# Optimization experiments

Hardware: AMD Instinct MI355X
Metric: run time of the kernel (lower is better)

## Reference

```python
import jax, jax.numpy as jnp
import numpy as np

EPS = 1e-6

B, R, S, CSEM = 4, 16384, 48, 4


def setup_inputs() -> dict:
    key = jax.random.key(0)
    k1, k2, k3, k4, k5 = jax.random.split(key, 5)
    colors = jax.random.uniform(k1, (B, R, S, 3), dtype=jnp.float32)
    densities = jax.random.normal(k2, (B, R, S, 1), dtype=jnp.float32)
    # depths must be monotonically increasing along the sample axis
    depths = jnp.sort(jax.random.uniform(k3, (B, R, S, 1), dtype=jnp.float32) * 5.0 + 0.5, axis=2)
    # semantics: per-sample class probabilities in [0,1]
    semantics = jax.nn.softmax(jax.random.normal(k4, (B, R, S, CSEM), dtype=jnp.float32), axis=-1)
    levels = jax.random.randint(k5, (B,), 0, 3, dtype=jnp.int32)
    return {"colors": colors, "densities": densities, "depths": depths,
            "semantics": semantics, "levels": levels}


def reference(colors, densities, depths, semantics, levels):
    dtype = colors.dtype
    # midpoints along the sample axis (dim 2)
    deltas = depths[:, :, 1:] - depths[:, :, :-1]            # [B,R,S-1,1]
    colors_mid = (colors[:, :, :-1] + colors[:, :, 1:]) * 0.5
    densities_mid = (densities[:, :, :-1] + densities[:, :, 1:]) * 0.5
    depths_mid = (depths[:, :, :-1] + depths[:, :, 1:]) * 0.5
    sem_mid = (semantics[:, :, :-1] + semantics[:, :, 1:]) * 0.5

    densities_mid = jax.nn.softplus(densities_mid).astype(dtype)  # activation_factory
    alpha = 1.0 - jnp.exp(-densities_mid * deltas)                # [B,R,S-1,1]

    # per-batch level masking (vectorized version of the python loop)
    lv = levels[:, None, None, None]                              # [B,1,1,1]
    sem0 = sem_mid[..., 0:1]
    sem3 = sem_mid[..., 3:4]
    factor = jnp.where(lv == 1, 1.0 - sem0,
             jnp.where(lv == 2, 1.0 - sem0 - sem3, 1.0))
    alpha = alpha * factor

    # level 1: zero ch0, renormalize ch1..3
    tail = sem_mid[..., 1:]
    sem_l1 = jnp.concatenate(
        [jnp.zeros_like(sem0), (tail + EPS) / (tail.sum(-1, keepdims=True) + EPS)], -1)
    # level 2: zero ch0 and ch3, renormalize ch1..2
    mid2 = sem_mid[..., 1:3]
    sem_l2 = jnp.concatenate(
        [jnp.zeros_like(sem0), (mid2 + EPS) / (mid2.sum(-1, keepdims=True) + EPS),
         jnp.zeros_like(sem3)], -1)
    sem_mid = jnp.where(lv == 1, sem_l1, jnp.where(lv == 2, sem_l2, sem_mid))

    # transmittance via exclusive cumprod along sample axis
    alpha_shifted = jnp.concatenate(
        [jnp.ones_like(alpha[:, :, :1]), 1.0 - alpha + 1e-10], axis=-2)
    weights = (alpha * jnp.cumprod(alpha_shifted, axis=-2)[:, :, :-1]).astype(dtype)

    composite_rgb = jnp.sum(weights * colors_mid, axis=-2)       # [B,R,3]
    composite_depth = jnp.sum(weights * depths_mid, axis=-2)     # [B,R,1]
    composite_semantics = jnp.sum(weights * sem_mid, axis=-2)    # [B,R,CSEM]

    composite_depth = jnp.where(jnp.isnan(composite_depth), jnp.inf, composite_depth).astype(dtype)
    composite_depth = jnp.clip(composite_depth, depths.min(), depths.max())
    return composite_rgb, composite_depth, composite_semantics, weights
```

## Files before the change

kernel.cpp:

```cpp
#include <hip/hip_runtime.h>
#include <math.h>

#define EPSF 1e-6f
#define NB 4
#define NR 16384
#define NS 48
#define NSEG 47
#define NRAYS (NB * NR)
#define KL 8
#define SPL 6
#define RPT 8
#define TPB 64
#define NBLK (NRAYS / RPT)

#define LC 0
#define LSM 1152
#define LD 2720
#define LZ 3104
#define LTOT 3496
#define LW LC
#define LP LSM

typedef const __attribute__((address_space(1))) void as1_cvoid;
typedef __attribute__((address_space(3))) void as3_void;

__device__ __forceinline__ float softplus_f(float x) {
    return fmaxf(x, 0.0f) + __logf(1.0f + __expf(-fabsf(x)));
}

__global__ __launch_bounds__(TPB) void march_kernel(
    const float* __restrict__ colors, const float* __restrict__ densities,
    const float* __restrict__ depths, const float* __restrict__ semantics,
    const int* __restrict__ levels, float2* __restrict__ ws2,
    float* __restrict__ out) {
    __shared__ float lds[LTOT];
    const int lane = threadIdx.x;
    const int r = lane >> 3;
    const int t = lane & 7;
    const int ray0 = blockIdx.x * RPT;
    const int ray = ray0 + r;
    const int lv = levels[ray >> 14];

    {
        const float* c = colors + (size_t)ray0 * 144;
#pragma unroll
        for (int i = 0; i < 4; ++i)
            __builtin_amdgcn_global_load_lds((as1_cvoid*)(c + i * 256 + lane * 4),
                                             (as3_void*)(lds + LC + i * 256), 16,
                                             0, 0);
        if (lane < 32)
            __builtin_amdgcn_global_load_lds((as1_cvoid*)(c + 1024 + lane * 4),
                                             (as3_void*)(lds + LC + 1024), 16, 0,
                                             0);
    }
    if (lane < 48) {
#pragma unroll
        for (int rr = 0; rr < 8; ++rr)
            __builtin_amdgcn_global_load_lds(
                (as1_cvoid*)(semantics + (size_t)(ray0 + rr) * 192 + lane * 4),
                (as3_void*)(lds + LSM + rr * 196), 16, 0, 0);
    }
    {
        const float* d = densities + (size_t)ray0 * 48;
        const float* z = depths + (size_t)ray0 * 48;
        __builtin_amdgcn_global_load_lds((as1_cvoid*)(d + lane * 4),
                                         (as3_void*)(lds + LD), 16, 0, 0);
        __builtin_amdgcn_global_load_lds((as1_cvoid*)(z + lane * 4),
                                         (as3_void*)(lds + LZ), 16, 0, 0);
        if (lane < 32) {
            __builtin_amdgcn_global_load_lds((as1_cvoid*)(d + 256 + lane * 4),
                                             (as3_void*)(lds + LD + 256), 16, 0,
                                             0);
            __builtin_amdgcn_global_load_lds((as1_cvoid*)(z + 256 + lane * 4),
                                             (as3_void*)(lds + LZ + 256), 16, 0,
                                             0);
        }
    }

    asm volatile("s_waitcnt vmcnt(0)" ::: "memory");

    {
        const int rr = lane & 7;
        float a = lds[LZ + rr * 48];
        float b = lds[LZ + rr * 48 + 47];
#pragma unroll
        for (int k = 1; k < 8; k <<= 1) {
            a = fminf(a, __shfl_xor(a, k));
            b = fmaxf(b, __shfl_xor(b, k));
        }
        if (lane == 0) ws2[blockIdx.x] = make_float2(a, b);
    }

    float C0[7], C1[7], C2[7], DN[7], Z[7], S0[7], S1[7], S2[7], S3[7];
    {
        const float* p0 = lds + LC + r * 144 + 18 * t;
        const float2* p = (const float2*)p0;
        float2 q0 = p[0], q1 = p[1], q2 = p[2], q3 = p[3], q4 = p[4];
        float2 q5 = p[5], q6 = p[6], q7 = p[7], q8 = p[8], q9 = p[9];
        float qa = p0[20];
        C0[0] = q0.x; C1[0] = q0.y; C2[0] = q1.x;
        C0[1] = q1.y; C1[1] = q2.x; C2[1] = q2.y;
        C0[2] = q3.x; C1[2] = q3.y; C2[2] = q4.x;
        C0[3] = q4.y; C1[3] = q5.x; C2[3] = q5.y;
        C0[4] = q6.x; C1[4] = q6.y; C2[4] = q7.x;
        C0[5] = q7.y; C1[5] = q8.x; C2[5] = q8.y;
        C0[6] = q9.x; C1[6] = q9.y; C2[6] = qa;
    }
    {
        const float4* p = (const float4*)(lds + LSM + r * 196 + 24 * t);
#pragma unroll
        for (int j = 0; j < 7; ++j) {
            float4 u = p[j];
            S0[j] = u.x; S1[j] = u.y; S2[j] = u.z; S3[j] = u.w;
        }
    }
    {
        const int dsel = (t < 7) ? 6 : 0;
        const int bd = LD + r * 48 + 6 * t;
        const float2* p = (const float2*)(lds + bd);
        float2 a0 = p[0], a1 = p[1], a2 = p[2];
        DN[0] = a0.x; DN[1] = a0.y; DN[2] = a1.x;
        DN[3] = a1.y; DN[4] = a2.x; DN[5] = a2.y;
        DN[6] = lds[bd + dsel];
        const int bz = LZ + r * 48 + 6 * t;
        const float2* q = (const float2*)(lds + bz);
        float2 b0 = q[0], b1 = q[1], b2 = q[2];
        Z[0] = b0.x; Z[1] = b0.y; Z[2] = b1.x;
        Z[3] = b1.y; Z[4] = b2.x; Z[5] = b2.y;
        Z[6] = lds[bz + dsel];
    }

    float T = 1.0f;
    float wl[SPL];
    float acc_r = 0.f, acc_g = 0.f, acc_b = 0.f, acc_d = 0.f;
    float acc_s0 = 0.f, acc_s1 = 0.f, acc_s2 = 0.f, acc_s3 = 0.f;

#pragma unroll
    for (int j = 0; j < SPL; ++j) {
        wl[j] = 0.0f;
        if (j < 5 || t < 7) {
            float delta = Z[j + 1] - Z[j];
            float cm0 = (C0[j] + C0[j + 1]) * 0.5f;
            float cm1 = (C1[j] + C1[j + 1]) * 0.5f;
            float cm2 = (C2[j] + C2[j + 1]) * 0.5f;
            float dnm = (DN[j] + DN[j + 1]) * 0.5f;
            float zm = (Z[j] + Z[j + 1]) * 0.5f;
            float sm0 = (S0[j] + S0[j + 1]) * 0.5f;
            float sm1 = (S1[j] + S1[j + 1]) * 0.5f;
            float sm2 = (S2[j] + S2[j + 1]) * 0.5f;
            float sm3 = (S3[j] + S3[j + 1]) * 0.5f;

            float sp_ = softplus_f(dnm);
            float alpha = 1.0f - __expf(-sp_ * delta);

            float factor, o0, o1, o2, o3;
            if (lv == 1) {
                factor = 1.0f - sm0;
                float inv = 1.0f / (sm1 + sm2 + sm3 + EPSF);
                o0 = 0.0f;
                o1 = (sm1 + EPSF) * inv;
                o2 = (sm2 + EPSF) * inv;
                o3 = (sm3 + EPSF) * inv;
            } else if (lv == 2) {
                factor = 1.0f - sm0 - sm3;
                float inv = 1.0f / (sm1 + sm2 + EPSF);
                o0 = 0.0f;
                o1 = (sm1 + EPSF) * inv;
                o2 = (sm2 + EPSF) * inv;
                o3 = 0.0f;
            } else {
                factor = 1.0f;
                o0 = sm0; o1 = sm1; o2 = sm2; o3 = sm3;
            }

            alpha *= factor;
            float w = alpha * T;
            T *= (1.0f - alpha + 1e-10f);
            wl[j] = w;

            acc_r += w * cm0;
            acc_g += w * cm1;
            acc_b += w * cm2;
            acc_d += w * zm;
            acc_s0 += w * o0;
            acc_s1 += w * o1;
            acc_s2 += w * o2;
            acc_s3 += w * o3;
        }
    }

    float p = T;
#pragma unroll
    for (int off = 1; off < KL; off <<= 1) {
        float u = __shfl_up(p, off, KL);
        if (t >= off) p *= u;
    }
    float Tstart = __shfl_up(p, 1, KL);
    if (t == 0) Tstart = 1.0f;

    acc_r *= Tstart; acc_g *= Tstart; acc_b *= Tstart; acc_d *= Tstart;
    acc_s0 *= Tstart; acc_s1 *= Tstart; acc_s2 *= Tstart; acc_s3 *= Tstart;

#pragma unroll
    for (int j = 0; j < SPL; ++j) {
        if (j < 5 || t < 7)
            lds[LW + r * NSEG + t * SPL + j] = wl[j] * Tstart;
    }

    {
        const int pb = LP + r * 72 + t * 9;
        lds[pb + 0] = acc_r;  lds[pb + 1] = acc_g;
        lds[pb + 2] = acc_b;  lds[pb + 3] = acc_d;
        lds[pb + 4] = acc_s0; lds[pb + 5] = acc_s1;
        lds[pb + 6] = acc_s2; lds[pb + 7] = acc_s3;
    }

    {
        const float4* src = (const float4*)(lds + LW);
        float4* dst = (float4*)(out + (size_t)NRAYS * 8 + (size_t)ray0 * NSEG);
        dst[lane] = src[lane];
        if (lane < 30) dst[64 + lane] = src[64 + lane];
    }

    {
        const int rr = lane >> 3, qq = lane & 7;
        const int qb = LP + rr * 72 + qq;
        float v = lds[qb] + lds[qb + 9];
        v += lds[qb + 18]; v += lds[qb + 27];
        v += lds[qb + 36]; v += lds[qb + 45];
        v += lds[qb + 54]; v += lds[qb + 63];

        const int oray = ray0 + rr;
        size_t oidx;
        if (qq < 3) {
            oidx = (size_t)oray * 3 + qq;
        } else if (qq == 3) {
            if (isnan(v)) v = INFINITY;
            oidx = (size_t)NRAYS * 3 + oray;
        } else {
            oidx = (size_t)NRAYS * 4 + (size_t)oray * 4 + (qq - 4);
        }
        out[oidx] = v;
    }
}

__global__ __launch_bounds__(256) void clip_depth(const float2* __restrict__ ws2,
                                                  float* __restrict__ dout) {
    __shared__ float smn[4], smx[4];
    float mn = INFINITY, mx = -INFINITY;
#pragma unroll
    for (int k = 0; k < 32; ++k) {
        float2 v = ws2[threadIdx.x + (k << 8)];
        mn = fminf(mn, v.x);
        mx = fmaxf(mx, v.y);
    }
#pragma unroll
    for (int off = 32; off > 0; off >>= 1) {
        mn = fminf(mn, __shfl_down(mn, off));
        mx = fmaxf(mx, __shfl_down(mx, off));
    }
    if ((threadIdx.x & 63) == 0) {
        smn[threadIdx.x >> 6] = mn;
        smx[threadIdx.x >> 6] = mx;
    }
    __syncthreads();
    mn = fminf(fminf(smn[0], smn[1]), fminf(smn[2], smn[3]));
    mx = fmaxf(fmaxf(smx[0], smx[1]), fmaxf(smx[2], smx[3]));

    float4* d4 = (float4*)dout;
    const int i = blockIdx.x * 256 + threadIdx.x;
    float4 v = d4[i];
    v.x = fminf(fmaxf(v.x, mn), mx);
    v.y = fminf(fmaxf(v.y, mn), mx);
    v.z = fminf(fmaxf(v.z, mn), mx);
    v.w = fminf(fmaxf(v.w, mn), mx);
    d4[i] = v;
}

extern "C" void kernel_launch(void* const* d_in, const int* in_sizes, int n_in,
                              void* d_out, int out_size, void* d_ws, size_t ws_size,
                              hipStream_t stream) {
    const float* colors = (const float*)d_in[0];
    const float* densities = (const float*)d_in[1];
    const float* depths = (const float*)d_in[2];
    const float* semantics = (const float*)d_in[3];
    const int* levels = (const int*)d_in[4];
    float* out = (float*)d_out;
    float2* ws2 = (float2*)d_ws;

    march_kernel<<<NBLK, TPB, 0, stream>>>(colors, densities, depths, semantics,
                                           levels, ws2, out);
    clip_depth<<<64, 256, 0, stream>>>(ws2, out + (size_t)NRAYS * 3);
}
```

Before: 30.10 us.

## Halve rays per block, stream samples from LDS, move depth min/max to separate kernel

```diff
diff --git a/kernel.cpp b/kernel.cpp
--- a/kernel.cpp
+++ b/kernel.cpp
@@ -7,17 +7,17 @@
 #define NS 48
 #define NSEG 47
 #define NRAYS (NB * NR)
-#define KL 8
-#define SPL 6
-#define RPT 8
+#define KL 16
+#define SPL 3
+#define RPT 4
 #define TPB 64
 #define NBLK (NRAYS / RPT)
 
 #define LC 0
-#define LSM 1152
-#define LD 2720
-#define LZ 3104
-#define LTOT 3496
+#define LSM 576
+#define LD 1360
+#define LZ 1552
+#define LTOT 1760
 #define LW LC
 #define LP LSM
 
@@ -28,107 +28,80 @@
     return fmaxf(x, 0.0f) + __logf(1.0f + __expf(-fabsf(x)));
 }
 
-__global__ __launch_bounds__(TPB) void march_kernel(
+__global__ __launch_bounds__(256) void minmax_ends(const float* __restrict__ z,
+                                                   float2* __restrict__ ws2) {
+    __shared__ float smn[4], smx[4];
+    float mn = INFINITY, mx = -INFINITY;
+#pragma unroll
+    for (int k = 0; k < 4; ++k) {
+        const int ray = blockIdx.x * 1024 + k * 256 + threadIdx.x;
+        mn = fminf(mn, z[(size_t)ray * NS]);
+        mx = fmaxf(mx, z[(size_t)ray * NS + (NS - 1)]);
+    }
+#pragma unroll
+    for (int off = 32; off > 0; off >>= 1) {
+        mn = fminf(mn, __shfl_down(mn, off));
+        mx = fmaxf(mx, __shfl_down(mx, off));
+    }
+    if ((threadIdx.x & 63) == 0) {
+        smn[threadIdx.x >> 6] = mn;
+        smx[threadIdx.x >> 6] = mx;
+    }
+    __syncthreads();
+    if (threadIdx.x == 0) {
+        mn = fminf(fminf(smn[0], smn[1]), fminf(smn[2], smn[3]));
+        mx = fmaxf(fmaxf(smx[0], smx[1]), fmaxf(smx[2], smx[3]));
+        ws2[blockIdx.x] = make_float2(mn, mx);
+    }
+}
+
+__global__ __launch_bounds__(TPB, 6) void march_kernel(
     const float* __restrict__ colors, const float* __restrict__ densities,
     const float* __restrict__ depths, const float* __restrict__ semantics,
-    const int* __restrict__ levels, float2* __restrict__ ws2,
-    float* __restrict__ out) {
+    const int* __restrict__ levels, float* __restrict__ out) {
     __shared__ float lds[LTOT];
     const int lane = threadIdx.x;
-    const int r = lane >> 3;
-    const int t = lane & 7;
+    const int r = lane >> 4;
+    const int t = lane & 15;
     const int ray0 = blockIdx.x * RPT;
     const int ray = ray0 + r;
     const int lv = levels[ray >> 14];
 
     {
         const float* c = colors + (size_t)ray0 * 144;
-#pragma unroll
-        for (int i = 0; i < 4; ++i)
-            __builtin_amdgcn_global_load_lds((as1_cvoid*)(c + i * 256 + lane * 4),
-                                             (as3_void*)(lds + LC + i * 256), 16,
-                                             0, 0);
-        if (lane < 32)
-            __builtin_amdgcn_global_load_lds((as1_cvoid*)(c + 1024 + lane * 4),
-                                             (as3_void*)(lds + LC + 1024), 16, 0,
+        __builtin_amdgcn_global_load_lds((as1_cvoid*)(c + lane * 4),
+                                         (as3_void*)(lds + LC), 16, 0, 0);
+        __builtin_amdgcn_global_load_lds((as1_cvoid*)(c + 256 + lane * 4),
+                                         (as3_void*)(lds + LC + 256), 16, 0, 0);
+        if (lane < 16)
+            __builtin_amdgcn_global_load_lds((as1_cvoid*)(c + 512 + lane * 4),
+                                             (as3_void*)(lds + LC + 512), 16, 0,
                                              0);
     }
     if (lane < 48) {
 #pragma unroll
-        for (int rr = 0; rr < 8; ++rr)
+        for (int rr = 0; rr < RPT; ++rr)
             __builtin_amdgcn_global_load_lds(
                 (as1_cvoid*)(semantics + (size_t)(ray0 + rr) * 192 + lane * 4),
                 (as3_void*)(lds + LSM + rr * 196), 16, 0, 0);
-    }
-    {
-        const float* d = densities + (size_t)ray0 * 48;
-        const float* z = depths + (size_t)ray0 * 48;
-        __builtin_amdgcn_global_load_lds((as1_cvoid*)(d + lane * 4),
-                                         (as3_void*)(lds + LD), 16, 0, 0);
-        __builtin_amdgcn_global_load_lds((as1_cvoid*)(z + lane * 4),
-                                         (as3_void*)(lds + LZ), 16, 0, 0);
-        if (lane < 32) {
-            __builtin_amdgcn_global_load_lds((as1_cvoid*)(d + 256 + lane * 4),
-                                             (as3_void*)(lds + LD + 256), 16, 0,
-                                             0);
-            __builtin_amdgcn_global_load_lds((as1_cvoid*)(z + 256 + lane * 4),
-                                             (as3_void*)(lds + LZ + 256), 16, 0,
-                                             0);
-        }
+        __builtin_amdgcn_global_load_lds(
+            (as1_cvoid*)(densities + (size_t)ray0 * 48 + lane * 4),
+            (as3_void*)(lds + LD), 16, 0, 0);
+        __builtin_amdgcn_global_load_lds(
+            (as1_cvoid*)(depths + (size_t)ray0 * 48 + lane * 4),
+            (as3_void*)(lds + LZ), 16, 0, 0);
     }
 
     asm volatile("s_waitcnt vmcnt(0)" ::: "memory");
 
-    {
-        const int rr = lane & 7;
-        float a = lds[LZ + rr * 48];
-        float b = lds[LZ + rr * 48 + 47];
-#pragma unroll
-        for (int k = 1; k < 8; k <<= 1) {
-            a = fminf(a, __shfl_xor(a, k));
-            b = fmaxf(b, __shfl_xor(b, k));
-        }
-        if (lane == 0) ws2[blockIdx.x] = make_float2(a, b);
-    }
-
-    float C0[7], C1[7], C2[7], DN[7], Z[7], S0[7], S1[7], S2[7], S3[7];
-    {
-        const float* p0 = lds + LC + r * 144 + 18 * t;
-        const float2* p = (const float2*)p0;
-        float2 q0 = p[0], q1 = p[1], q2 = p[2], q3 = p[3], q4 = p[4];
-        float2 q5 = p[5], q6 = p[6], q7 = p[7], q8 = p[8], q9 = p[9];
-        float qa = p0[20];
-        C0[0] = q0.x; C1[0] = q0.y; C2[0] = q1.x;
-        C0[1] = q1.y; C1[1] = q2.x; C2[1] = q2.y;
-        C0[2] = q3.x; C1[2] = q3.y; C2[2] = q4.x;
-        C0[3] = q4.y; C1[3] = q5.x; C2[3] = q5.y;
-        C0[4] = q6.x; C1[4] = q6.y; C2[4] = q7.x;
-        C0[5] = q7.y; C1[5] = q8.x; C2[5] = q8.y;
-        C0[6] = q9.x; C1[6] = q9.y; C2[6] = qa;
-    }
-    {
-        const float4* p = (const float4*)(lds + LSM + r * 196 + 24 * t);
-#pragma unroll
-        for (int j = 0; j < 7; ++j) {
-            float4 u = p[j];
-            S0[j] = u.x; S1[j] = u.y; S2[j] = u.z; S3[j] = u.w;
-        }
-    }
-    {
-        const int dsel = (t < 7) ? 6 : 0;
-        const int bd = LD + r * 48 + 6 * t;
-        const float2* p = (const float2*)(lds + bd);
-        float2 a0 = p[0], a1 = p[1], a2 = p[2];
-        DN[0] = a0.x; DN[1] = a0.y; DN[2] = a1.x;
-        DN[3] = a1.y; DN[4] = a2.x; DN[5] = a2.y;
-        DN[6] = lds[bd + dsel];
-        const int bz = LZ + r * 48 + 6 * t;
-        const float2* q = (const float2*)(lds + bz);
-        float2 b0 = q[0], b1 = q[1], b2 = q[2];
-        Z[0] = b0.x; Z[1] = b0.y; Z[2] = b1.x;
-        Z[3] = b1.y; Z[4] = b2.x; Z[5] = b2.y;
-        Z[6] = lds[bz + dsel];
-    }
+    const int cb = LC + r * 144 + 9 * t;
+    const float4* sp = (const float4*)(lds + LSM + r * 196);
+    const int db = LD + r * 48 + 3 * t;
+    const int zb = LZ + r * 48 + 3 * t;
+
+    float pc0 = lds[cb + 0], pc1 = lds[cb + 1], pc2 = lds[cb + 2];
+    float4 psm = sp[3 * t];
+    float pdn = lds[db], pz = lds[zb];
 
     float T = 1.0f;
     float wl[SPL];
@@ -137,18 +110,25 @@
 
 #pragma unroll
     for (int j = 0; j < SPL; ++j) {
+        float c0 = lds[cb + 3 * (j + 1)];
+        float c1 = lds[cb + 3 * (j + 1) + 1];
+        float c2 = lds[cb + 3 * (j + 1) + 2];
+        float4 sm4 = sp[3 * t + j + 1];
+        float dn = lds[db + j + 1];
+        float z = lds[zb + j + 1];
+
         wl[j] = 0.0f;
-        if (j < 5 || t < 7) {
-            float delta = Z[j + 1] - Z[j];
-            float cm0 = (C0[j] + C0[j + 1]) * 0.5f;
-            float cm1 = (C1[j] + C1[j + 1]) * 0.5f;
-            float cm2 = (C2[j] + C2[j + 1]) * 0.5f;
-            float dnm = (DN[j] + DN[j + 1]) * 0.5f;
-            float zm = (Z[j] + Z[j + 1]) * 0.5f;
-            float sm0 = (S0[j] + S0[j + 1]) * 0.5f;
-            float sm1 = (S1[j] + S1[j + 1]) * 0.5f;
-            float sm2 = (S2[j] + S2[j + 1]) * 0.5f;
-            float sm3 = (S3[j] + S3[j + 1]) * 0.5f;
+        if (j < 2 || t < 15) {
+            float delta = z - pz;
+            float cm0 = (pc0 + c0) * 0.5f;
+            float cm1 = (pc1 + c1) * 0.5f;
+            float cm2 = (pc2 + c2) * 0.5f;
+            float dnm = (pdn + dn) * 0.5f;
+            float zm = (pz + z) * 0.5f;
+            float sm0 = (psm.x + sm4.x) * 0.5f;
+            float sm1 = (psm.y + sm4.y) * 0.5f;
+            float sm2 = (psm.z + sm4.z) * 0.5f;
+            float sm3 = (psm.w + sm4.w) * 0.5f;
 
             float sp_ = softplus_f(dnm);
             float alpha = 1.0f - __expf(-sp_ * delta);
@@ -187,6 +167,8 @@
             acc_s2 += w * o2;
             acc_s3 += w * o3;
         }
+        pc0 = c0; pc1 = c1; pc2 = c2;
+        psm = sm4; pdn = dn; pz = z;
     }
 
     float p = T;
@@ -203,32 +185,30 @@
 
 #pragma unroll
     for (int j = 0; j < SPL; ++j) {
-        if (j < 5 || t < 7)
-            lds[LW + r * NSEG + t * SPL + j] = wl[j] * Tstart;
+        if (j < 2 || t < 15)
+            lds[LW + r * NSEG + 3 * t + j] = wl[j] * Tstart;
     }
 
     {
-        const int pb = LP + r * 72 + t * 9;
+        const int pb = LP + r * 144 + t * 9;
         lds[pb + 0] = acc_r;  lds[pb + 1] = acc_g;
         lds[pb + 2] = acc_b;  lds[pb + 3] = acc_d;
         lds[pb + 4] = acc_s0; lds[pb + 5] = acc_s1;
         lds[pb + 6] = acc_s2; lds[pb + 7] = acc_s3;
     }
 
-    {
+    if (lane < 47) {
         const float4* src = (const float4*)(lds + LW);
         float4* dst = (float4*)(out + (size_t)NRAYS * 8 + (size_t)ray0 * NSEG);
         dst[lane] = src[lane];
-        if (lane < 30) dst[64 + lane] = src[64 + lane];
-    }
-
-    {
+    }
+
+    if (lane < 32) {
         const int rr = lane >> 3, qq = lane & 7;
-        const int qb = LP + rr * 72 + qq;
-        float v = lds[qb] + lds[qb + 9];
-        v += lds[qb + 18]; v += lds[qb + 27];
-        v += lds[qb + 36]; v += lds[qb + 45];
-        v += lds[qb + 54]; v += lds[qb + 63];
+        const int qb = LP + rr * 144 + qq;
+        float v = 0.0f;
+#pragma unroll
+        for (int k = 0; k < KL; ++k) v += lds[qb + 9 * k];
 
         const int oray = ray0 + rr;
         size_t oidx;
@@ -248,11 +228,10 @@
                                                   float* __restrict__ dout) {
     __shared__ float smn[4], smx[4];
     float mn = INFINITY, mx = -INFINITY;
-#pragma unroll
-    for (int k = 0; k < 32; ++k) {
-        float2 v = ws2[threadIdx.x + (k << 8)];
-        mn = fminf(mn, v.x);
-        mx = fmaxf(mx, v.y);
+    if (threadIdx.x < 64) {
+        float2 v = ws2[threadIdx.x];
+        mn = v.x;
+        mx = v.y;
     }
 #pragma unroll
     for (int off = 32; off > 0; off >>= 1) {
@@ -288,7 +267,8 @@
     float* out = (float*)d_out;
     float2* ws2 = (float2*)d_ws;
 
+    minmax_ends<<<64, 256, 0, stream>>>(depths, ws2);
     march_kernel<<<NBLK, TPB, 0, stream>>>(colors, densities, depths, semantics,
-                                           levels, ws2, out);
+                                           levels, out);
     clip_depth<<<64, 256, 0, stream>>>(ws2, out + (size_t)NRAYS * 3);
 }
```

Result: slower. 32.80 us (+9.0%).
